# Optimization experiments

Hardware: AMD Instinct MI355X
Metric: run time of the kernel (lower is better)

## Reference

```python
import jax, jax.numpy as jnp
import numpy as np

N_NODES = 100000
N_EDGES = 1600000
D_IN = 128
D_OUT = 128


def setup_inputs() -> dict:
    key = jax.random.key(0)
    k1, k2, k3 = jax.random.split(key, 3)
    x = jax.random.normal(k1, (N_NODES, D_IN), dtype=jnp.float32)
    edge_index = jax.random.randint(k2, (2, N_EDGES), 0, N_NODES, dtype=jnp.int32)
    W = jax.random.normal(k3, (D_IN, D_OUT), dtype=jnp.float32) / np.sqrt(D_IN)
    b = jnp.zeros((D_OUT,), dtype=jnp.float32)
    return {"x": x, "edge_index": edge_index, "W": W, "b": b}


def reference(x, edge_index, W, b):
    """GCNConv (add self-loops, symmetric norm) + ReLU.
    out = relu(D^-1/2 (A+I) D^-1/2 X W + b)
    """
    N = x.shape[0]
    src, dst = edge_index[0], edge_index[1]
    loop = jnp.arange(N, dtype=src.dtype)
    src = jnp.concatenate([src, loop])  # [E+N]
    dst = jnp.concatenate([dst, loop])  # [E+N]

    # degree of target nodes (includes self-loop, so deg >= 1)
    deg = jax.ops.segment_sum(jnp.ones(dst.shape, dtype=x.dtype), dst,
                              num_segments=N)
    deg_inv_sqrt = jax.lax.rsqrt(deg)
    norm = deg_inv_sqrt[src] * deg_inv_sqrt[dst]  # [E+N]

    h = x @ W  # [N, D_OUT] — transform before aggregation (PyG GCNConv)
    msg = h[src] * norm[:, None]  # gather + normalize
    out = jax.ops.segment_sum(msg, dst, num_segments=N)  # scatter-add
    return jax.nn.relu(out + b)
```

## Files before the change

kernel.cpp:

```cpp
#include <hip/hip_runtime.h>

#define N_NODES 100000
#define N_EDGES 1600000
#define D 128
#define SUBW 32
#define NSUB2 3125
#define NC 196
#define BSH 9
#define BMSK 511
#define CAPC 12288
#define CAP3 9728
#define CAPS2 1024
#define CHUNK3 4096
#define BIND_BLOCKS ((N_EDGES + CHUNK3 - 1) / CHUNK3)
#define GEMM2_BLOCKS ((N_NODES + 127) / 128)
#define STAGE_MAX (CHUNK3 + NC * 16)
#define NGRP (STAGE_MAX / 16)
#define CCSTRIDE 16

typedef __attribute__((ext_vector_type(8))) short short8;
typedef __attribute__((ext_vector_type(4))) float float4v;

__device__ inline unsigned short f2bf(float f) {
    unsigned u = __float_as_uint(f);
    unsigned r = (u + 0x7fffu + ((u >> 16) & 1u)) >> 16;
    return (unsigned short)r;
}
__device__ inline float bflo(unsigned int p) { return __uint_as_float(p << 16); }
__device__ inline float bfhi(unsigned int p) { return __uint_as_float(p & 0xffff0000u); }

__global__ void probe_convert_kernel(const unsigned int* __restrict__ xw,
                                     const void* __restrict__ b,
                                     const void* __restrict__ Wv,
                                     int* __restrict__ flag, float* __restrict__ bfv,
                                     unsigned short* __restrict__ Wbf,
                                     int* __restrict__ ccnt) {
    __shared__ int cnt;
    if (threadIdx.x == 0) cnt = 0;
    __syncthreads();
    unsigned low = xw[threadIdx.x] & 0xFFFFu;
    unsigned e = (low >> 7) & 0xFFu;
    atomicAdd(&cnt, (int)((e == 0u) || (e >= 107u && e <= 147u)));
    __syncthreads();
    int m = (cnt >= 192);
    if (threadIdx.x == 0) *flag = m;
    if (threadIdx.x < D)
        bfv[threadIdx.x] = m ? bflo(((const unsigned short*)b)[threadIdx.x])
                             : ((const float*)b)[threadIdx.x];
    for (int i = threadIdx.x; i < D * D; i += 256)
        Wbf[i] = m ? ((const unsigned short*)Wv)[i] : f2bf(((const float*)Wv)[i]);
    for (int i = threadIdx.x; i < NC * CCSTRIDE; i += 256) ccnt[i] = 0;
}

__global__ void __launch_bounds__(256) binD_kernel(
        const int* __restrict__ src, const int* __restrict__ dst,
        int* __restrict__ ccnt, unsigned* __restrict__ recg) {
    __shared__ __align__(16) unsigned stg[STAGE_MAX];
    __shared__ int cnt[NC], cpad[NC], ofs[NC], base[NC], place[NC];
    __shared__ unsigned short g2b[NGRP];
    __shared__ int tot;

    int tid = threadIdx.x;
    int e0 = blockIdx.x * CHUNK3;
    int e1 = e0 + CHUNK3 < N_EDGES ? e0 + CHUNK3 : N_EDGES;
    if (tid < NC) cnt[tid] = 0;
    __syncthreads();

    unsigned recs[16];
    int bks[16];
    #pragma unroll
    for (int k = 0; k < 4; ++k) {
        int i = e0 + tid * 4 + k * 1024;
        if (i + 3 < e1) {
            int4 d4 = *(const int4*)&dst[i];
            int4 s4 = *(const int4*)&src[i];
            recs[k * 4 + 0] = (unsigned)s4.x | ((unsigned)(d4.x & BMSK) << 17); bks[k * 4 + 0] = d4.x >> BSH;
            recs[k * 4 + 1] = (unsigned)s4.y | ((unsigned)(d4.y & BMSK) << 17); bks[k * 4 + 1] = d4.y >> BSH;
            recs[k * 4 + 2] = (unsigned)s4.z | ((unsigned)(d4.z & BMSK) << 17); bks[k * 4 + 2] = d4.z >> BSH;
            recs[k * 4 + 3] = (unsigned)s4.w | ((unsigned)(d4.w & BMSK) << 17); bks[k * 4 + 3] = d4.w >> BSH;
        } else {
            bks[k * 4 + 0] = -1; bks[k * 4 + 1] = -1; bks[k * 4 + 2] = -1; bks[k * 4 + 3] = -1;
            recs[k * 4 + 0] = 0; recs[k * 4 + 1] = 0; recs[k * 4 + 2] = 0; recs[k * 4 + 3] = 0;
        }
    }
    #pragma unroll
    for (int k = 0; k < 16; ++k)
        if (bks[k] >= 0) atomicAdd(&cnt[bks[k]], 1);
    __syncthreads();

    if (tid < NC) {
        int c = cnt[tid];
        int p = (c + 15) & ~15;
        cpad[tid] = p;
        base[tid] = p ? atomicAdd(&ccnt[tid * CCSTRIDE], p) : 0;
    }
    __syncthreads();
    if (tid == 0) {
        int s = 0;
        for (int k = 0; k < NC; ++k) { ofs[k] = s; place[k] = s; s += cpad[k]; }
        tot = s;
    }
    __syncthreads();
    if (tid < NC) {
        int o = ofs[tid], e = o + cpad[tid];
        for (int j = o + cnt[tid]; j < e; ++j) stg[j] = 0xFFFFFFFFu;
        for (int g = o >> 4; g < (e >> 4); ++g) g2b[g] = (unsigned short)tid;
    }
    __syncthreads();

    #pragma unroll
    for (int k = 0; k < 16; ++k)
        if (bks[k] >= 0) {
            int p = atomicAdd(&place[bks[k]], 1);
            stg[p] = recs[k];
        }
    __syncthreads();

    int tot_ = tot;
    for (int j = tid * 4; j < tot_; j += 1024) {
        int lo = g2b[j >> 4];
        int gi = base[lo] + (j - ofs[lo]);
        if (gi < CAPC)
            *(uint4*)&recg[(size_t)lo * CAPC + gi] = *(const uint4*)&stg[j];
    }
}

__global__ void __launch_bounds__(512) fused_sortgemm_kernel(
        unsigned* __restrict__ recg, const int* __restrict__ ccnt,
        int* __restrict__ deg, int* __restrict__ nodeofs, float* __restrict__ dis,
        const void* __restrict__ xv, const unsigned short* __restrict__ Wbf,
        const int* __restrict__ flag, unsigned short* __restrict__ h) {
    __shared__ union {
        struct {
            int hist[512], ofs[512], place[512], wsum[8];
            __align__(16) unsigned s_srt[CAP3];
        } s;
        unsigned short Wt[D * 136];
    } u;

    int tid = threadIdx.x;

    if (blockIdx.x < NC) {
        int b = blockIdx.x;
        u.s.hist[tid] = 0;
        __syncthreads();
        int count = ccnt[b * CCSTRIDE]; if (count > CAPC) count = CAPC;
        const unsigned* r = recg + (size_t)b * CAPC;
        for (int i = tid * 4; i + 3 < count; i += 2048) {
            uint4 w4 = *(const uint4*)&r[i];
            if (w4.x != 0xFFFFFFFFu) atomicAdd(&u.s.hist[w4.x >> 17], 1);
            if (w4.y != 0xFFFFFFFFu) atomicAdd(&u.s.hist[w4.y >> 17], 1);
            if (w4.z != 0xFFFFFFFFu) atomicAdd(&u.s.hist[w4.z >> 17], 1);
            if (w4.w != 0xFFFFFFFFu) atomicAdd(&u.s.hist[w4.w >> 17], 1);
        }
        __syncthreads();

        int lane = tid & 63, wave = tid >> 6;
        int h0 = u.s.hist[tid];
        int v = h0;
        #pragma unroll
        for (int dsh = 1; dsh < 64; dsh <<= 1) {
            int uu = __shfl_up(v, dsh);
            if (lane >= dsh) v += uu;
        }
        if (lane == 63) u.s.wsum[wave] = v;
        __syncthreads();
        int wbase = 0;
        #pragma unroll
        for (int k = 0; k < 8; ++k) if (k < wave) wbase += u.s.wsum[k];
        int e0v = wbase + v - h0;
        u.s.ofs[tid] = e0v; u.s.place[tid] = e0v;
        int n = b * 512 + tid;
        deg[n] = h0;
        nodeofs[n] = e0v;
        dis[n] = rsqrtf((float)(h0 + 1));
        __syncthreads();

        for (int i = tid * 4; i + 3 < count; i += 2048) {
            uint4 w4 = *(const uint4*)&r[i];
            if (w4.x != 0xFFFFFFFFu) { int p = atomicAdd(&u.s.place[w4.x >> 17], 1); if (p < CAP3) u.s.s_srt[p] = w4.x & 0x1FFFFu; }
            if (w4.y != 0xFFFFFFFFu) { int p = atomicAdd(&u.s.place[w4.y >> 17], 1); if (p < CAP3) u.s.s_srt[p] = w4.y & 0x1FFFFu; }
            if (w4.z != 0xFFFFFFFFu) { int p = atomicAdd(&u.s.place[w4.z >> 17], 1); if (p < CAP3) u.s.s_srt[p] = w4.z & 0x1FFFFu; }
            if (w4.w != 0xFFFFFFFFu) { int p = atomicAdd(&u.s.place[w4.w >> 17], 1); if (p < CAP3) u.s.s_srt[p] = w4.w & 0x1FFFFu; }
        }
        __syncthreads();

        int total = u.s.ofs[511] + u.s.hist[511];
        int totR = (total + 15) & ~15; if (totR > CAP3) totR = CAP3;
        unsigned* w = recg + (size_t)b * CAPC;
        for (int j = tid * 4; j < totR; j += 2048)
            *(uint4*)&w[j] = *(const uint4*)&u.s.s_srt[j];
    } else {
        int bid2 = blockIdx.x - NC;
        int m = *flag;
        for (int idx = tid; idx < D * D; idx += 512) {
            int k = idx >> 7, c = idx & 127;
            u.Wt[c * 136 + k] = Wbf[idx];
        }
        __syncthreads();

        int wave = tid >> 6, lane = tid & 63;
        int row0 = (bid2 * 8 + wave) * 16;
        if (row0 >= N_NODES) return;
        int r = lane & 15, quad = lane >> 4;

        short8 a[4];
        if (m) {
            const unsigned short* xr = (const unsigned short*)xv + (size_t)(row0 + r) * D + quad * 8;
            #pragma unroll
            for (int t = 0; t < 4; ++t) a[t] = *(const short8*)(xr + t * 32);
        } else {
            const float* xr = (const float*)xv + (size_t)(row0 + r) * D + quad * 8;
            #pragma unroll
            for (int t = 0; t < 4; ++t) {
                float4 f0 = *(const float4*)(xr + t * 32);
                float4 f1 = *(const float4*)(xr + t * 32 + 4);
                a[t][0] = (short)f2bf(f0.x); a[t][1] = (short)f2bf(f0.y);
                a[t][2] = (short)f2bf(f0.z); a[t][3] = (short)f2bf(f0.w);
                a[t][4] = (short)f2bf(f1.x); a[t][5] = (short)f2bf(f1.y);
                a[t][6] = (short)f2bf(f1.z); a[t][7] = (short)f2bf(f1.w);
            }
        }

        #pragma unroll
        for (int ct = 0; ct < 8; ++ct) {
            int col0 = ct * 16;
            float4v c = {0.f, 0.f, 0.f, 0.f};
            #pragma unroll
            for (int t = 0; t < 4; ++t) {
                short8 bfr = *(const short8*)&u.Wt[(col0 + r) * 136 + t * 32 + quad * 8];
                c = __builtin_amdgcn_mfma_f32_16x16x32_bf16(a[t], bfr, c, 0, 0, 0);
            }
            #pragma unroll
            for (int reg = 0; reg < 4; ++reg) {
                int orow = row0 + quad * 4 + reg;
                h[(size_t)orow * D + col0 + r] = f2bf(c[reg]);
            }
        }
    }
}

__global__ void __launch_bounds__(256) agg5_kernel(
        const unsigned* __restrict__ srt2, const int* __restrict__ nodeofs,
        const int* __restrict__ deg, const float* __restrict__ dis,
        const float* __restrict__ bfv, const int* __restrict__ flag,
        const unsigned short* __restrict__ h, void* __restrict__ out) {
    __shared__ unsigned srt[CAPS2];
    __shared__ int l_ofs[SUBW];
    __shared__ int l_deg[SUBW];
    __shared__ float lbias[D];

    int sub = blockIdx.x, tid = threadIdx.x;
    int n0 = sub * SUBW;
    int B = n0 >> BSH, loc0 = n0 & BMSK;
    if (tid < SUBW) {
        l_ofs[tid] = nodeofs[B * 512 + loc0 + tid];
        l_deg[tid] = deg[n0 + tid];
    }
    if (tid < D) lbias[tid] = bfv[tid];
    __syncthreads();

    int base0 = l_ofs[0];
    int span = (l_ofs[SUBW - 1] + l_deg[SUBW - 1]) - base0;
    if (span > CAPS2) span = CAPS2;
    if (span > CAP3 - base0) span = CAP3 - base0;
    const unsigned* sb = srt2 + (size_t)B * CAPC + base0;
    for (int i = tid; i < span; i += 256) srt[i] = sb[i];
    __syncthreads();

    const uint4* h4 = (const uint4*)h;
    int wave = tid >> 6, lane = tid & 63;
    int q = lane >> 4, c16 = lane & 15;
    int m = *flag;

    for (int t = 0; t < 8; ++t) {
        int nl = wave * 8 + t;
        int n = n0 + nl;
        int o = l_ofs[nl] - base0;
        int cnt = l_deg[nl];
        int e_end = o + cnt; if (e_end > span) e_end = span;

        uint4 sp = make_uint4(0u, 0u, 0u, 0u);
        if (q == 0) sp = h4[(size_t)n * 16 + c16];

        float acc[8] = {0.f, 0.f, 0.f, 0.f, 0.f, 0.f, 0.f, 0.f};
        int j = o + q;
        for (; j + 4 < e_end; j += 8) {
            unsigned s0 = srt[j];
            unsigned s1 = srt[j + 4];
            uint4 p0 = h4[(size_t)s0 * 16 + c16];
            uint4 p1 = h4[(size_t)s1 * 16 + c16];
            float w0 = dis[s0], w1 = dis[s1];
            acc[0] += w0 * bflo(p0.x); acc[1] += w0 * bfhi(p0.x);
            acc[2] += w0 * bflo(p0.y); acc[3] += w0 * bfhi(p0.y);
            acc[4] += w0 * bflo(p0.z); acc[5] += w0 * bfhi(p0.z);
            acc[6] += w0 * bflo(p0.w); acc[7] += w0 * bfhi(p0.w);
            acc[0] += w1 * bflo(p1.x); acc[1] += w1 * bfhi(p1.x);
            acc[2] += w1 * bflo(p1.y); acc[3] += w1 * bfhi(p1.y);
            acc[4] += w1 * bflo(p1.z); acc[5] += w1 * bfhi(p1.z);
            acc[6] += w1 * bflo(p1.w); acc[7] += w1 * bfhi(p1.w);
        }
        if (j < e_end) {
            unsigned s0 = srt[j];
            uint4 p0 = h4[(size_t)s0 * 16 + c16];
            float w0 = dis[s0];
            acc[0] += w0 * bflo(p0.x); acc[1] += w0 * bfhi(p0.x);
            acc[2] += w0 * bflo(p0.y); acc[3] += w0 * bfhi(p0.y);
            acc[4] += w0 * bflo(p0.z); acc[5] += w0 * bfhi(p0.z);
            acc[6] += w0 * bflo(p0.w); acc[7] += w0 * bfhi(p0.w);
        }
        #pragma unroll
        for (int i = 0; i < 8; ++i) {
            acc[i] += __shfl_xor(acc[i], 16);
            acc[i] += __shfl_xor(acc[i], 32);
        }

        if (q == 0) {
            float dn = rsqrtf((float)(cnt + 1));
            float v[8];
            v[0] = fmaxf(dn * (acc[0] + dn * bflo(sp.x)) + lbias[c16 * 8 + 0], 0.f);
            v[1] = fmaxf(dn * (acc[1] + dn * bfhi(sp.x)) + lbias[c16 * 8 + 1], 0.f);
            v[2] = fmaxf(dn * (acc[2] + dn * bflo(sp.y)) + lbias[c16 * 8 + 2], 0.f);
            v[3] = fmaxf(dn * (acc[3] + dn * bfhi(sp.y)) + lbias[c16 * 8 + 3], 0.f);
            v[4] = fmaxf(dn * (acc[4] + dn * bflo(sp.z)) + lbias[c16 * 8 + 4], 0.f);
            v[5] = fmaxf(dn * (acc[5] + dn * bfhi(sp.z)) + lbias[c16 * 8 + 5], 0.f);
            v[6] = fmaxf(dn * (acc[6] + dn * bflo(sp.w)) + lbias[c16 * 8 + 6], 0.f);
            v[7] = fmaxf(dn * (acc[7] + dn * bfhi(sp.w)) + lbias[c16 * 8 + 7], 0.f);
            if (m) {
                uint4 pk;
                pk.x = ((unsigned)f2bf(v[1]) << 16) | f2bf(v[0]);
                pk.y = ((unsigned)f2bf(v[3]) << 16) | f2bf(v[2]);
                pk.z = ((unsigned)f2bf(v[5]) << 16) | f2bf(v[4]);
                pk.w = ((unsigned)f2bf(v[7]) << 16) | f2bf(v[6]);
                ((uint4*)out)[(size_t)n * 16 + c16] = pk;
            } else {
                float4 f0 = make_float4(v[0], v[1], v[2], v[3]);
                float4 f1 = make_float4(v[4], v[5], v[6], v[7]);
                float4* of = (float4*)((float*)out + (size_t)n * D + c16 * 8);
                of[0] = f0; of[1] = f1;
            }
        }
    }
}

extern "C" void kernel_launch(void* const* d_in, const int* in_sizes, int n_in,
                              void* d_out, int out_size, void* d_ws, size_t ws_size,
                              hipStream_t stream) {
    const void* x = nullptr; const int* ei = nullptr;
    const void* W = nullptr; const void* b = nullptr;
    for (int i = 0; i < n_in; ++i) {
        if      (in_sizes[i] == N_NODES * D) x  = d_in[i];
        else if (in_sizes[i] == 2 * N_EDGES) ei = (const int*)d_in[i];
        else if (in_sizes[i] == D * D)       W  = d_in[i];
        else if (in_sizes[i] == D)           b  = d_in[i];
    }
    if (!x || !ei || !W || !b) {
        x = d_in[0]; ei = (const int*)d_in[1]; W = d_in[2]; b = d_in[3];
    }
    const int* src = ei;
    const int* dst = ei + N_EDGES;

    char* ws = (char*)d_ws;
    int*      flag    = (int*)ws;
    int*      ccnt    = (int*)(ws + 16);
    float*    bfv     = (float*)(ccnt + NC * CCSTRIDE);
    unsigned short* Wbf = (unsigned short*)(bfv + D);
    int*      deg     = (int*)(Wbf + D * D);
    int*      nodeofs = deg + NC * 512;
    float*    dis     = (float*)(nodeofs + NC * 512);
    unsigned* recg    = (unsigned*)(dis + NC * 512);
    unsigned short* h = (unsigned short*)(recg + (size_t)NC * CAPC);

    probe_convert_kernel<<<1, 256, 0, stream>>>((const unsigned int*)x, b, W,
                                                flag, bfv, Wbf, ccnt);

    binD_kernel<<<BIND_BLOCKS, 256, 0, stream>>>(src, dst, ccnt, recg);

    fused_sortgemm_kernel<<<NC + GEMM2_BLOCKS, 512, 0, stream>>>(
        recg, ccnt, deg, nodeofs, dis, x, Wbf, flag, h);

    agg5_kernel<<<NSUB2, 256, 0, stream>>>(recg, nodeofs, deg, dis, bfv, flag, h, d_out);
}
```

Before: 242.9 us.

## Split GEMM across binning and sort kernels to overlap with edge binning

Moves half of the X·W GEMM blocks into the edge-binning kernel, which now runs at 512 threads per block, and keeps the other half alongside the per-bucket sort kernel, so compute-heavy GEMM work overlaps with the memory- and atomic-bound binning and sorting stages. It also swaps the MFMA operand order so each lane writes four contiguous bf16 outputs as one packed 8-byte store instead of scattered 2-byte stores. The binning shared memory now shares a union with the W tile, which may lower occupancy for the binning blocks. Load balance between the two halves depends on the fixed block split.

```diff
diff --git a/kernel.cpp b/kernel.cpp
--- a/kernel.cpp
+++ b/kernel.cpp
@@ -13,7 +13,8 @@
 #define CAPS2 1024
 #define CHUNK3 4096
 #define BIND_BLOCKS ((N_EDGES + CHUNK3 - 1) / CHUNK3)
-#define GEMM2_BLOCKS ((N_NODES + 127) / 128)
+#define GEMMH_BLOCKS 391
+#define ROWS_HALF (GEMMH_BLOCKS * 128)
 #define STAGE_MAX (CHUNK3 + NC * 16)
 #define NGRP (STAGE_MAX / 16)
 #define CCSTRIDE 16
@@ -52,80 +53,140 @@
     for (int i = threadIdx.x; i < NC * CCSTRIDE; i += 256) ccnt[i] = 0;
 }
 
-__global__ void __launch_bounds__(256) binD_kernel(
+__device__ inline void gemm_block(const void* __restrict__ xv,
+                                  const unsigned short* __restrict__ Wbf,
+                                  int m, unsigned short* __restrict__ h,
+                                  unsigned short* Wt, int tid, int row_block0) {
+    for (int idx = tid; idx < D * D; idx += 512) {
+        int k = idx >> 7, c = idx & 127;
+        Wt[c * 136 + k] = Wbf[idx];
+    }
+    __syncthreads();
+
+    int wave = tid >> 6, lane = tid & 63;
+    int row0 = row_block0 + wave * 16;
+    if (row0 >= N_NODES) return;
+    int r = lane & 15, quad = lane >> 4;
+
+    short8 a[4];
+    if (m) {
+        const unsigned short* xr = (const unsigned short*)xv + (size_t)(row0 + r) * D + quad * 8;
+        #pragma unroll
+        for (int t = 0; t < 4; ++t) a[t] = *(const short8*)(xr + t * 32);
+    } else {
+        const float* xr = (const float*)xv + (size_t)(row0 + r) * D + quad * 8;
+        #pragma unroll
+        for (int t = 0; t < 4; ++t) {
+            float4 f0 = *(const float4*)(xr + t * 32);
+            float4 f1 = *(const float4*)(xr + t * 32 + 4);
+            a[t][0] = (short)f2bf(f0.x); a[t][1] = (short)f2bf(f0.y);
+            a[t][2] = (short)f2bf(f0.z); a[t][3] = (short)f2bf(f0.w);
+            a[t][4] = (short)f2bf(f1.x); a[t][5] = (short)f2bf(f1.y);
+            a[t][6] = (short)f2bf(f1.z); a[t][7] = (short)f2bf(f1.w);
+        }
+    }
+
+    #pragma unroll
+    for (int ct = 0; ct < 8; ++ct) {
+        int col0 = ct * 16;
+        float4v c4 = {0.f, 0.f, 0.f, 0.f};
+        #pragma unroll
+        for (int t = 0; t < 4; ++t) {
+            short8 bfr = *(const short8*)&Wt[(col0 + r) * 136 + t * 32 + quad * 8];
+            c4 = __builtin_amdgcn_mfma_f32_16x16x32_bf16(bfr, a[t], c4, 0, 0, 0);
+        }
+        unsigned u0 = (unsigned)f2bf(c4[0]) | ((unsigned)f2bf(c4[1]) << 16);
+        unsigned u1 = (unsigned)f2bf(c4[2]) | ((unsigned)f2bf(c4[3]) << 16);
+        *(uint2*)&h[(size_t)(row0 + r) * D + col0 + quad * 4] = make_uint2(u0, u1);
+    }
+}
+
+__global__ void __launch_bounds__(512) fused_bin_gemmA_kernel(
         const int* __restrict__ src, const int* __restrict__ dst,
-        int* __restrict__ ccnt, unsigned* __restrict__ recg) {
-    __shared__ __align__(16) unsigned stg[STAGE_MAX];
-    __shared__ int cnt[NC], cpad[NC], ofs[NC], base[NC], place[NC];
-    __shared__ unsigned short g2b[NGRP];
-    __shared__ int tot;
+        int* __restrict__ ccnt, unsigned* __restrict__ recg,
+        const void* __restrict__ xv, const unsigned short* __restrict__ Wbf,
+        const int* __restrict__ flag, unsigned short* __restrict__ h) {
+    __shared__ union {
+        struct {
+            __align__(16) unsigned stg[STAGE_MAX];
+            int cnt[NC], cpad[NC], ofs[NC], base[NC], place[NC];
+            unsigned short g2b[NGRP];
+            int tot;
+        } b;
+        unsigned short Wt[D * 136];
+    } u;
 
     int tid = threadIdx.x;
-    int e0 = blockIdx.x * CHUNK3;
-    int e1 = e0 + CHUNK3 < N_EDGES ? e0 + CHUNK3 : N_EDGES;
-    if (tid < NC) cnt[tid] = 0;
-    __syncthreads();
-
-    unsigned recs[16];
-    int bks[16];
-    #pragma unroll
-    for (int k = 0; k < 4; ++k) {
-        int i = e0 + tid * 4 + k * 1024;
-        if (i + 3 < e1) {
-            int4 d4 = *(const int4*)&dst[i];
-            int4 s4 = *(const int4*)&src[i];
-            recs[k * 4 + 0] = (unsigned)s4.x | ((unsigned)(d4.x & BMSK) << 17); bks[k * 4 + 0] = d4.x >> BSH;
-            recs[k * 4 + 1] = (unsigned)s4.y | ((unsigned)(d4.y & BMSK) << 17); bks[k * 4 + 1] = d4.y >> BSH;
-            recs[k * 4 + 2] = (unsigned)s4.z | ((unsigned)(d4.z & BMSK) << 17); bks[k * 4 + 2] = d4.z >> BSH;
-            recs[k * 4 + 3] = (unsigned)s4.w | ((unsigned)(d4.w & BMSK) << 17); bks[k * 4 + 3] = d4.w >> BSH;
-        } else {
-            bks[k * 4 + 0] = -1; bks[k * 4 + 1] = -1; bks[k * 4 + 2] = -1; bks[k * 4 + 3] = -1;
-            recs[k * 4 + 0] = 0; recs[k * 4 + 1] = 0; recs[k * 4 + 2] = 0; recs[k * 4 + 3] = 0;
-        }
-    }
-    #pragma unroll
-    for (int k = 0; k < 16; ++k)
-        if (bks[k] >= 0) atomicAdd(&cnt[bks[k]], 1);
-    __syncthreads();
-
-    if (tid < NC) {
-        int c = cnt[tid];
-        int p = (c + 15) & ~15;
-        cpad[tid] = p;
-        base[tid] = p ? atomicAdd(&ccnt[tid * CCSTRIDE], p) : 0;
-    }
-    __syncthreads();
-    if (tid == 0) {
-        int s = 0;
-        for (int k = 0; k < NC; ++k) { ofs[k] = s; place[k] = s; s += cpad[k]; }
-        tot = s;
-    }
-    __syncthreads();
-    if (tid < NC) {
-        int o = ofs[tid], e = o + cpad[tid];
-        for (int j = o + cnt[tid]; j < e; ++j) stg[j] = 0xFFFFFFFFu;
-        for (int g = o >> 4; g < (e >> 4); ++g) g2b[g] = (unsigned short)tid;
-    }
-    __syncthreads();
-
-    #pragma unroll
-    for (int k = 0; k < 16; ++k)
-        if (bks[k] >= 0) {
-            int p = atomicAdd(&place[bks[k]], 1);
-            stg[p] = recs[k];
-        }
-    __syncthreads();
-
-    int tot_ = tot;
-    for (int j = tid * 4; j < tot_; j += 1024) {
-        int lo = g2b[j >> 4];
-        int gi = base[lo] + (j - ofs[lo]);
-        if (gi < CAPC)
-            *(uint4*)&recg[(size_t)lo * CAPC + gi] = *(const uint4*)&stg[j];
-    }
-}
-
-__global__ void __launch_bounds__(512) fused_sortgemm_kernel(
+
+    if (blockIdx.x < BIND_BLOCKS) {
+        int e0 = blockIdx.x * CHUNK3;
+        int e1 = e0 + CHUNK3 < N_EDGES ? e0 + CHUNK3 : N_EDGES;
+        if (tid < NC) u.b.cnt[tid] = 0;
+        __syncthreads();
+
+        unsigned recs[8];
+        int bks[8];
+        #pragma unroll
+        for (int k = 0; k < 2; ++k) {
+            int i = e0 + tid * 4 + k * 2048;
+            if (i + 3 < e1) {
+                int4 d4 = *(const int4*)&dst[i];
+                int4 s4 = *(const int4*)&src[i];
+                recs[k * 4 + 0] = (unsigned)s4.x | ((unsigned)(d4.x & BMSK) << 17); bks[k * 4 + 0] = d4.x >> BSH;
+                recs[k * 4 + 1] = (unsigned)s4.y | ((unsigned)(d4.y & BMSK) << 17); bks[k * 4 + 1] = d4.y >> BSH;
+                recs[k * 4 + 2] = (unsigned)s4.z | ((unsigned)(d4.z & BMSK) << 17); bks[k * 4 + 2] = d4.z >> BSH;
+                recs[k * 4 + 3] = (unsigned)s4.w | ((unsigned)(d4.w & BMSK) << 17); bks[k * 4 + 3] = d4.w >> BSH;
+            } else {
+                bks[k * 4 + 0] = -1; bks[k * 4 + 1] = -1; bks[k * 4 + 2] = -1; bks[k * 4 + 3] = -1;
+                recs[k * 4 + 0] = 0; recs[k * 4 + 1] = 0; recs[k * 4 + 2] = 0; recs[k * 4 + 3] = 0;
+            }
+        }
+        #pragma unroll
+        for (int k = 0; k < 8; ++k)
+            if (bks[k] >= 0) atomicAdd(&u.b.cnt[bks[k]], 1);
+        __syncthreads();
+
+        if (tid < NC) {
+            int c = u.b.cnt[tid];
+            int p = (c + 15) & ~15;
+            u.b.cpad[tid] = p;
+            u.b.base[tid] = p ? atomicAdd(&ccnt[tid * CCSTRIDE], p) : 0;
+        }
+        __syncthreads();
+        if (tid == 0) {
+            int s = 0;
+            for (int k = 0; k < NC; ++k) { u.b.ofs[k] = s; u.b.place[k] = s; s += u.b.cpad[k]; }
+            u.b.tot = s;
+        }
+        __syncthreads();
+        if (tid < NC) {
+            int o = u.b.ofs[tid], e = o + u.b.cpad[tid];
+            for (int j = o + u.b.cnt[tid]; j < e; ++j) u.b.stg[j] = 0xFFFFFFFFu;
+            for (int g = o >> 4; g < (e >> 4); ++g) u.b.g2b[g] = (unsigned short)tid;
+        }
+        __syncthreads();
+
+        #pragma unroll
+        for (int k = 0; k < 8; ++k)
+            if (bks[k] >= 0) {
+                int p = atomicAdd(&u.b.place[bks[k]], 1);
+                u.b.stg[p] = recs[k];
+            }
+        __syncthreads();
+
+        int tot_ = u.b.tot;
+        for (int j = tid * 4; j < tot_; j += 2048) {
+            int lo = u.b.g2b[j >> 4];
+            int gi = u.b.base[lo] + (j - u.b.ofs[lo]);
+            if (gi < CAPC)
+                *(uint4*)&recg[(size_t)lo * CAPC + gi] = *(const uint4*)&u.b.stg[j];
+        }
+    } else {
+        gemm_block(xv, Wbf, *flag, h, u.Wt, tid, (int)(blockIdx.x - BIND_BLOCKS) * 128);
+    }
+}
+
+__global__ void __launch_bounds__(512) fused_sort_gemmB_kernel(
         unsigned* __restrict__ recg, const int* __restrict__ ccnt,
         int* __restrict__ deg, int* __restrict__ nodeofs, float* __restrict__ dis,
         const void* __restrict__ xv, const unsigned short* __restrict__ Wbf,
@@ -191,52 +252,8 @@
         for (int j = tid * 4; j < totR; j += 2048)
             *(uint4*)&w[j] = *(const uint4*)&u.s.s_srt[j];
     } else {
-        int bid2 = blockIdx.x - NC;
-        int m = *flag;
-        for (int idx = tid; idx < D * D; idx += 512) {
-            int k = idx >> 7, c = idx & 127;
-            u.Wt[c * 136 + k] = Wbf[idx];
-        }
-        __syncthreads();
-
-        int wave = tid >> 6, lane = tid & 63;
-        int row0 = (bid2 * 8 + wave) * 16;
-        if (row0 >= N_NODES) return;
-        int r = lane & 15, quad = lane >> 4;
-
-        short8 a[4];
-        if (m) {
-            const unsigned short* xr = (const unsigned short*)xv + (size_t)(row0 + r) * D + quad * 8;
-            #pragma unroll
-            for (int t = 0; t < 4; ++t) a[t] = *(const short8*)(xr + t * 32);
-        } else {
-            const float* xr = (const float*)xv + (size_t)(row0 + r) * D + quad * 8;
-            #pragma unroll
-            for (int t = 0; t < 4; ++t) {
-                float4 f0 = *(const float4*)(xr + t * 32);
-                float4 f1 = *(const float4*)(xr + t * 32 + 4);
-                a[t][0] = (short)f2bf(f0.x); a[t][1] = (short)f2bf(f0.y);
-                a[t][2] = (short)f2bf(f0.z); a[t][3] = (short)f2bf(f0.w);
-                a[t][4] = (short)f2bf(f1.x); a[t][5] = (short)f2bf(f1.y);
-                a[t][6] = (short)f2bf(f1.z); a[t][7] = (short)f2bf(f1.w);
-            }
-        }
-
-        #pragma unroll
-        for (int ct = 0; ct < 8; ++ct) {
-            int col0 = ct * 16;
-            float4v c = {0.f, 0.f, 0.f, 0.f};
-            #pragma unroll
-            for (int t = 0; t < 4; ++t) {
-                short8 bfr = *(const short8*)&u.Wt[(col0 + r) * 136 + t * 32 + quad * 8];
-                c = __builtin_amdgcn_mfma_f32_16x16x32_bf16(a[t], bfr, c, 0, 0, 0);
-            }
-            #pragma unroll
-            for (int reg = 0; reg < 4; ++reg) {
-                int orow = row0 + quad * 4 + reg;
-                h[(size_t)orow * D + col0 + r] = f2bf(c[reg]);
-            }
-        }
+        gemm_block(xv, Wbf, *flag, h, u.Wt, tid,
+                   ROWS_HALF + (int)(blockIdx.x - NC) * 128);
     }
 }
 
@@ -374,9 +391,10 @@
     probe_convert_kernel<<<1, 256, 0, stream>>>((const unsigned int*)x, b, W,
                                                 flag, bfv, Wbf, ccnt);
 
-    binD_kernel<<<BIND_BLOCKS, 256, 0, stream>>>(src, dst, ccnt, recg);
-
-    fused_sortgemm_kernel<<<NC + GEMM2_BLOCKS, 512, 0, stream>>>(
+    fused_bin_gemmA_kernel<<<BIND_BLOCKS + GEMMH_BLOCKS, 512, 0, stream>>>(
+        src, dst, ccnt, recg, x, Wbf, flag, h);
+
+    fused_sort_gemmB_kernel<<<NC + GEMMH_BLOCKS, 512, 0, stream>>>(
         recg, ccnt, deg, nodeofs, dis, x, Wbf, flag, h);
 
     agg5_kernel<<<NSUB2, 256, 0, stream>>>(recg, nodeofs, deg, dis, bfv, flag, h, d_out);
```

Result: no change. 242.4 us (-0.2%).
